# Optimization experiments

Hardware: AMD Instinct MI355X
Metric: run time of the kernel (lower is better)

Reference implementation:

```python
import jax, jax.numpy as jnp
import numpy as np

B, S, D, E, H = 1024, 256, 1024, 1024, 1024  # batch, state, belief, embedding, hidden
T1 = 32            # clip_length => number of scan steps
POSE_TILES = 4
MIN_STD = 0.1


def _gru(x, h, wih, whh, bih, bhh):
    # torch.nn.GRUCell semantics
    gi = x @ wih.T + bih
    gh = h @ whh.T + bhh
    i_r, i_z, i_n = jnp.split(gi, 3, axis=-1)
    h_r, h_z, h_n = jnp.split(gh, 3, axis=-1)
    r = jax.nn.sigmoid(i_r + h_r)
    z = jax.nn.sigmoid(i_z + h_z)
    n = jnp.tanh(i_n + r * h_n)
    return (1.0 - z) * n + z * h


def setup_inputs() -> dict:
    key = jax.random.key(0)
    ks = iter(jax.random.split(key, 40))
    g = lambda shape, s=1.0: jax.random.normal(next(ks), shape, dtype=jnp.float32) * s
    W = 0.02
    inp = {
        'prev_state': g((B, S)),
        'prev_belief': g((B, D)),
        'observations': g((T1, B, E)),
        'poses': g((T1, B, 6)),
        'noise_post': g((T1, B, S)),
        'noise_prior': g((T1, B, S)),
        # fc_embed_state_posterior: (2S+E) -> D
        'W_esq': g((D, 2 * S + E), W), 'b_esq': jnp.zeros((D,), jnp.float32),
        # fc_embed_state_prior: (2S+6*pose_tiles) -> D
        'W_esp': g((D, 2 * S + 6 * POSE_TILES), W), 'b_esp': jnp.zeros((D,), jnp.float32),
        # GRUCell posterior / prior
        'gq_wih': g((3 * D, D), W), 'gq_whh': g((3 * D, D), W),
        'gq_bih': jnp.zeros((3 * D,), jnp.float32), 'gq_bhh': jnp.zeros((3 * D,), jnp.float32),
        'gp_wih': g((3 * D, D), W), 'gp_whh': g((3 * D, D), W),
        'gp_bih': jnp.zeros((3 * D,), jnp.float32), 'gp_bhh': jnp.zeros((3 * D,), jnp.float32),
        # belief -> hidden -> 2*state heads
        'W_ebq': g((H, D), W), 'b_ebq': jnp.zeros((H,), jnp.float32),
        'W_sq': g((2 * S, H), W), 'b_sq': jnp.zeros((2 * S,), jnp.float32),
        'W_ebp': g((H, D), W), 'b_ebp': jnp.zeros((H,), jnp.float32),
        'W_sp': g((2 * S, H), W), 'b_sp': jnp.zeros((2 * S,), jnp.float32),
    }
    return inp


def reference(prev_state, prev_belief, observations, poses, noise_post, noise_prior,
              W_esq, b_esq, W_esp, b_esp,
              gq_wih, gq_whh, gq_bih, gq_bhh,
              gp_wih, gp_whh, gp_bih, gp_bhh,
              W_ebq, b_ebq, W_sq, b_sq, W_ebp, b_ebp, W_sp, b_sp):
    relu = jax.nn.relu

    def step(carry, xs):
        s_q, s_p, b_q, b_p = carry
        obs, pose, nq, npn = xs
        # posterior branch
        h = relu(jnp.concatenate([obs, s_q, s_p], axis=1) @ W_esq.T + b_esq)
        b_q_new = _gru(h, b_q, gq_wih, gq_whh, gq_bih, gq_bhh)
        hq = relu(b_q_new @ W_ebq.T + b_ebq)
        mq, raw_sq = jnp.split(hq @ W_sq.T + b_sq, 2, axis=1)
        std_q = jax.nn.softplus(raw_sq) + MIN_STD
        s_q_new = mq + std_q * nq
        # prior branch (uses old s_q, s_p per original code)
        pose_t = jnp.tile(pose, (1, POSE_TILES))
        h2 = relu(jnp.concatenate([pose_t, s_q, s_p], axis=1) @ W_esp.T + b_esp)
        b_p_new = _gru(h2, b_p, gp_wih, gp_whh, gp_bih, gp_bhh)
        hp = relu(b_p_new @ W_ebp.T + b_ebp)
        mp, raw_sp = jnp.split(hp @ W_sp.T + b_sp, 2, axis=1)
        std_p = jax.nn.softplus(raw_sp) + MIN_STD
        s_p_new = mp + std_p * npn
        new_carry = (s_q_new, s_p_new, b_q_new, b_p_new)
        ys = (b_q_new, s_p_new, mp, std_p, s_q_new, mq, std_q)
        return new_carry, ys

    carry0 = (prev_state, prev_state, prev_belief, prev_belief)
    _, ys = jax.lax.scan(step, carry0, (observations, poses, noise_post, noise_prior))
    post_beliefs, prior_states, prior_means, prior_stds, post_states, post_means, post_stds = ys
    # order matches torch: [posterior_beliefs, prior_states, prior_means, prior_std_devs,
    #                       posterior_states, posterior_means, posterior_std_devs]
    return (post_beliefs, prior_states, prior_means, prior_stds,
            post_states, post_means, post_stds)
```

## Files before the change

### kernel.cpp

```cpp
#include <hip/hip_runtime.h>
#include <stdint.h>
#include <math.h>

typedef unsigned short ushort_t;
typedef __attribute__((ext_vector_type(8))) short bf16x8;
typedef __attribute__((ext_vector_type(4))) float f32x4;

#define T1_ 32

#define SW_BAR() asm volatile("s_barrier" ::: "memory")
#define SW_VM(n) asm volatile("s_waitcnt vmcnt(" #n ")" ::: "memory")

__device__ __forceinline__ float bf2f(ushort_t u) {
  union { unsigned int i; float f; } v; v.i = ((unsigned int)u) << 16; return v.f;
}
__device__ __forceinline__ ushort_t f2bf(float f) {
  union { float f; unsigned int i; } v; v.f = f;
  unsigned int x = v.i;
  return (ushort_t)((x + 0x7FFFu + ((x >> 16) & 1u)) >> 16);
}
__device__ __forceinline__ float sigm(float x) { return 1.f / (1.f + expf(-x)); }

__device__ __forceinline__ void gld16(const ushort_t* g, ushort_t* l) {
  __builtin_amdgcn_global_load_lds(
      (const __attribute__((address_space(1))) unsigned int*)g,
      (__attribute__((address_space(3))) unsigned int*)l, 16, 0, 0);
}


__global__ __launch_bounds__(256) void cvt_k(const float* src, ushort_t* dst,
                                             long long n, int cols, int src_ld, int src_off) {
  const long long idx = (long long)blockIdx.x * 256 + threadIdx.x;
  if (idx >= n) return;
  const long long row = idx / cols;
  const int col = (int)(idx - row * cols);
  dst[idx] = f2bf(src[row * src_ld + src_off + col]);
}

__global__ __launch_bounds__(256) void wpe_k(const float* Wesp, float* wpe) {
  const int i = blockIdx.x * 256 + threadIdx.x;
  if (i >= 1024 * 6) return;
  const int n = i / 6, j = i % 6;
  float s = 0.f;
#pragma unroll
  for (int r = 0; r < 4; ++r) s += Wesp[(long long)n * 536 + j + 6 * r];
  wpe[i] = s;
}

__global__ void marker_k(float* out, float K) {
  if (threadIdx.x == 0 && blockIdx.x == 0) out[0] = K;
}

struct ObsqArgs { const ushort_t* A; const ushort_t* W; ushort_t* out; };
__global__ __launch_bounds__(256) void obsq_k(ObsqArgs g) {
  __shared__ __align__(16) ushort_t As[2][2048];
  __shared__ __align__(16) ushort_t Ws[2][4096];
  const int tid = threadIdx.x;
  const int lane = tid & 63, wv = tid >> 6;
  const int wm = wv >> 1, wn = wv & 1;
  const int bn0 = blockIdx.x * 128, bm0 = blockIdx.y * 64;
  const int srow = lane >> 2;
  const int sch8 = ((lane ^ (lane >> 2) ^ (lane >> 4)) & 3) * 8;
  const int rr = lane & 15, qq = lane >> 4;
  const int rslot8 = (((rr << 2) | ((qq ^ rr ^ (rr >> 2)) & 3)) * 8);

  f32x4 acc[2][4];
#pragma unroll
  for (int i = 0; i < 2; ++i)
#pragma unroll
    for (int j = 0; j < 4; ++j) acc[i][j] = (f32x4){0.f, 0.f, 0.f, 0.f};

  auto stage = [&](int buf, int kt) {
    const int k0 = kt * 32;
    gld16(g.A + (size_t)(bm0 + wv * 16 + srow) * 1024 + k0 + sch8, &As[buf][wv * 512]);
    gld16(g.W + (size_t)(bn0 + wv * 16 + srow) * 1536 + k0 + sch8, &Ws[buf][wv * 512]);
    gld16(g.W + (size_t)(bn0 + 64 + wv * 16 + srow) * 1536 + k0 + sch8,
          &Ws[buf][2048 + wv * 512]);
  };

  stage(0, 0);
  int cur = 0;
#pragma unroll 1
  for (int kt = 0; kt < 32; ++kt) {
    if (kt + 1 < 32) { stage(cur ^ 1, kt + 1); SW_VM(3); } else { SW_VM(0); }
    SW_BAR();
    bf16x8 a[2], b[4];
#pragma unroll
    for (int i = 0; i < 2; ++i)
      a[i] = *(const bf16x8*)&As[cur][(wm * 2 + i) * 512 + rslot8];
#pragma unroll
    for (int j = 0; j < 4; ++j)
      b[j] = *(const bf16x8*)&Ws[cur][(wn * 4 + j) * 512 + rslot8];
#pragma unroll
    for (int i = 0; i < 2; ++i)
#pragma unroll
      for (int j = 0; j < 4; ++j)
        acc[i][j] = __builtin_amdgcn_mfma_f32_16x16x32_bf16(a[i], b[j], acc[i][j], 0, 0, 0);
    if (kt + 1 < 32) SW_BAR();
    cur ^= 1;
  }

  const int r15 = lane & 15, rq = (lane >> 4) * 4;
#pragma unroll
  for (int i = 0; i < 2; ++i)
#pragma unroll
    for (int j = 0; j < 4; ++j) {
      const int col = bn0 + wn * 64 + j * 16 + r15;
#pragma unroll
      for (int q = 0; q < 4; ++q) {
        const int row = bm0 + wm * 32 + i * 16 + rq + q;
        g.out[(size_t)row * 1024 + col] = f2bf(acc[i][j][q]);
      }
    }
}

struct MMSide {
  const ushort_t* a0; const ushort_t* a1; const ushort_t* a2;
  int kd0, kd1, kd2;
  int coff0, coff1, coff2;
  const ushort_t* W; int ldw;
  const float* bias;
  ushort_t* outb;
  int dopose;
  const ushort_t* extrab;
};
struct MM2Args { MMSide s[2]; const float* poses_t; const float* wpe; };

__global__ __launch_bounds__(256) void mm2_k(MM2Args g) {
  const MMSide S = g.s[blockIdx.z];
  __shared__ __align__(16) ushort_t As[2][1024];
  __shared__ __align__(16) ushort_t Ws[2][4096];
  const int tid = threadIdx.x;
  const int lane = tid & 63, wv = tid >> 6;
  const int wn = wv;
  const int bn0 = blockIdx.x * 128, bm0 = blockIdx.y * 32;
  const int srow = lane >> 2;
  const int sch8 = ((lane ^ (lane >> 2) ^ (lane >> 4)) & 3) * 8;
  const int rr = lane & 15, qq = lane >> 4;
  const int rslot8 = (((rr << 2) | ((qq ^ rr ^ (rr >> 2)) & 3)) * 8);

  f32x4 acc[2][2];
#pragma unroll
  for (int i = 0; i < 2; ++i)
#pragma unroll
    for (int j = 0; j < 2; ++j) acc[i][j] = (f32x4){0.f, 0.f, 0.f, 0.f};

  const int nk0 = S.kd0 >> 5, nk1 = S.kd1 >> 5, nk2 = S.kd2 >> 5;
  const int c1 = nk0, c2 = nk0 + nk1, nkt = c2 + nk2;

  auto stage = [&](int buf, int ktg) {
    const ushort_t* ab; int ktl, kdim, cf;
    if (ktg < c1)      { ab = S.a0; ktl = ktg;      kdim = S.kd0; cf = S.coff0; }
    else if (ktg < c2) { ab = S.a1; ktl = ktg - c1; kdim = S.kd1; cf = S.coff1; }
    else               { ab = S.a2; ktl = ktg - c2; kdim = S.kd2; cf = S.coff2; }
    const int k0 = ktl * 32;
    gld16(S.W + cf + (size_t)(bn0 + wv * 16 + srow) * S.ldw + k0 + sch8, &Ws[buf][wv * 512]);
    gld16(S.W + cf + (size_t)(bn0 + 64 + wv * 16 + srow) * S.ldw + k0 + sch8,
          &Ws[buf][(wv + 4) * 512]);
    if (wv < 2)
      gld16(ab + (size_t)(bm0 + wv * 16 + srow) * kdim + k0 + sch8, &As[buf][wv * 512]);
  };

  stage(0, 0);
  int cur = 0;
#pragma unroll 1
  for (int ktg = 0; ktg < nkt; ++ktg) {
    if (ktg + 1 < nkt) {
      stage(cur ^ 1, ktg + 1);
      if (wv < 2) { SW_VM(3); } else { SW_VM(2); }
    } else { SW_VM(0); }
    SW_BAR();
    bf16x8 a[2], b[2];
#pragma unroll
    for (int i = 0; i < 2; ++i)
      a[i] = *(const bf16x8*)&As[cur][i * 512 + rslot8];
#pragma unroll
    for (int j = 0; j < 2; ++j)
      b[j] = *(const bf16x8*)&Ws[cur][(wn * 2 + j) * 512 + rslot8];
#pragma unroll
    for (int i = 0; i < 2; ++i)
#pragma unroll
      for (int j = 0; j < 2; ++j)
        acc[i][j] = __builtin_amdgcn_mfma_f32_16x16x32_bf16(a[i], b[j], acc[i][j], 0, 0, 0);
    if (ktg + 1 < nkt) SW_BAR();
    cur ^= 1;
  }

  const int r15 = lane & 15, rq = (lane >> 4) * 4;
#pragma unroll
  for (int i = 0; i < 2; ++i) {
#pragma unroll
    for (int j = 0; j < 2; ++j) {
      const int col = bn0 + wn * 32 + j * 16 + r15;
      const float bs = S.bias[col];
#pragma unroll
      for (int q = 0; q < 4; ++q) {
        const int row = bm0 + i * 16 + rq + q;
        float v = acc[i][j][q] + bs;
        if (S.extrab) v += bf2f(S.extrab[(size_t)row * 1024 + col]);
        if (S.dopose) {
          float s = 0.f;
#pragma unroll
          for (int jj = 0; jj < 6; ++jj)
            s += g.poses_t[(long long)row * 6 + jj] * g.wpe[col * 6 + jj];
          v += s;
        }
        v = fmaxf(v, 0.f);
        S.outb[(size_t)row * 1024 + col] = f2bf(v);
      }
    }
  }
}

struct GruSide {
  const ushort_t* x;
  const ushort_t* hb;
  const float* hf;
  const ushort_t* wih; const ushort_t* whh;
  const float* bih; const float* bhh;
  float* dst; ushort_t* dstb;
};
struct Gru2Args { GruSide s[2]; };

__global__ __launch_bounds__(256) void gru2_k(Gru2Args g) {
  const GruSide S = g.s[blockIdx.z];
  __shared__ __align__(16) ushort_t lds[2][16384];
  const int tid = threadIdx.x;
  const int lane = tid & 63, wv = tid >> 6;
  const int wm = wv >> 1, wn = wv & 1;
  const int bn0 = blockIdx.x * 64, bm0 = blockIdx.y * 64;
  const int srow = lane >> 2;
  const int sch8 = ((lane ^ (lane >> 2) ^ (lane >> 4)) & 3) * 8;
  const int rr = lane & 15, qq = lane >> 4;
  const int rslot8 = (((rr << 2) | ((qq ^ rr ^ (rr >> 2)) & 3)) * 8);

  f32x4 aR[2][2], aZ[2][2], aNI[2][2], aNH[2][2];
#pragma unroll
  for (int i = 0; i < 2; ++i)
#pragma unroll
    for (int j = 0; j < 2; ++j) {
      aR[i][j] = (f32x4){0.f,0.f,0.f,0.f}; aZ[i][j] = (f32x4){0.f,0.f,0.f,0.f};
      aNI[i][j] = (f32x4){0.f,0.f,0.f,0.f}; aNH[i][j] = (f32x4){0.f,0.f,0.f,0.f};
    }

  auto stage = [&](int buf, int kt) {
    const int k0 = kt * 32;
#pragma unroll
    for (int u = 0; u < 8; ++u) {
      const int G = wv * 8 + u;
      if (G < 4)
        gld16(S.x + (size_t)(bm0 + G * 16 + srow) * 1024 + k0 + sch8, &lds[buf][G * 512]);
      else if (G < 8)
        gld16(S.hb + (size_t)(bm0 + (G - 4) * 16 + srow) * 1024 + k0 + sch8, &lds[buf][G * 512]);
      else {
        const int wch = G - 8, gg = wch >> 2, rc = wch & 3;
        const ushort_t* base = (gg < 3) ? S.wih : S.whh;
        const int gr = (gg < 3 ? gg : gg - 3) * 1024 + bn0 + rc * 16 + srow;
        gld16(base + (size_t)gr * 1024 + k0 + sch8, &lds[buf][G * 512]);
      }
    }
  };

  stage(0, 0);
  int cur = 0;
#pragma unroll 1
  for (int kt = 0; kt < 32; ++kt) {
    if (kt + 1 < 32) { stage(cur ^ 1, kt + 1); SW_VM(8); } else { SW_VM(0); }
    SW_BAR();
    bf16x8 ax[2], ah[2], w[6][2];
#pragma unroll
    for (int i = 0; i < 2; ++i) {
      ax[i] = *(const bf16x8*)&lds[cur][(wm * 2 + i) * 512 + rslot8];
      ah[i] = *(const bf16x8*)&lds[cur][(4 + wm * 2 + i) * 512 + rslot8];
    }
#pragma unroll
    for (int gg = 0; gg < 6; ++gg)
#pragma unroll
      for (int j = 0; j < 2; ++j)
        w[gg][j] = *(const bf16x8*)&lds[cur][(8 + gg * 4 + wn * 2 + j) * 512 + rslot8];
#pragma unroll
    for (int i = 0; i < 2; ++i)
#pragma unroll
      for (int j = 0; j < 2; ++j) {
        aR[i][j]  = __builtin_amdgcn_mfma_f32_16x16x32_bf16(ax[i], w[0][j], aR[i][j], 0, 0, 0);
        aR[i][j]  = __builtin_amdgcn_mfma_f32_16x16x32_bf16(ah[i], w[3][j], aR[i][j], 0, 0, 0);
        aZ[i][j]  = __builtin_amdgcn_mfma_f32_16x16x32_bf16(ax[i], w[1][j], aZ[i][j], 0, 0, 0);
        aZ[i][j]  = __builtin_amdgcn_mfma_f32_16x16x32_bf16(ah[i], w[4][j], aZ[i][j], 0, 0, 0);
        aNI[i][j] = __builtin_amdgcn_mfma_f32_16x16x32_bf16(ax[i], w[2][j], aNI[i][j], 0, 0, 0);
        aNH[i][j] = __builtin_amdgcn_mfma_f32_16x16x32_bf16(ah[i], w[5][j], aNH[i][j], 0, 0, 0);
      }
    if (kt + 1 < 32) SW_BAR();
    cur ^= 1;
  }

  const int r15 = lane & 15, rq = (lane >> 4) * 4;
#pragma unroll
  for (int j = 0; j < 2; ++j) {
    const int col = bn0 + wn * 32 + j * 16 + r15;
    const float brz = S.bih[col] + S.bhh[col];
    const float bzz = S.bih[col + 1024] + S.bhh[col + 1024];
    const float bni = S.bih[col + 2048], bnh = S.bhh[col + 2048];
#pragma unroll
    for (int i = 0; i < 2; ++i) {
#pragma unroll
      for (int q = 0; q < 4; ++q) {
        const int row = bm0 + wm * 32 + i * 16 + rq + q;
        const float r = sigm(aR[i][j][q] + brz);
        const float z = sigm(aZ[i][j][q] + bzz);
        const float ng = tanhf(aNI[i][j][q] + bni + r * (aNH[i][j][q] + bnh));
        const size_t o = (size_t)row * 1024 + col;
        const float bnew = (1.f - z) * ng + z * S.hf[o];
        S.dst[o] = bnew;
        S.dstb[o] = f2bf(bnew);
      }
    }
  }
}

struct HeadSide {
  const ushort_t* hh;
  const ushort_t* Ws;
  const float* bs;
  const float* noise;
  float* omean; float* ostd; float* ostate;
  ushort_t* stateb;
};
struct Head2Args { HeadSide s[2]; };

__global__ __launch_bounds__(256) void head2_k(Head2Args g) {
  const HeadSide S = g.s[blockIdx.z];
  __shared__ __align__(16) ushort_t lds[2][3072];
  const int tid = threadIdx.x;
  const int lane = tid & 63, wv = tid >> 6;
  const int wm = wv >> 1, wn = wv & 1;
  const int bn0 = blockIdx.x * 32, bm0 = blockIdx.y * 32;
  const int srow = lane >> 2;
  const int sch8 = ((lane ^ (lane >> 2) ^ (lane >> 4)) & 3) * 8;
  const int rr = lane & 15, qq = lane >> 4;
  const int rslot8 = (((rr << 2) | ((qq ^ rr ^ (rr >> 2)) & 3)) * 8);

  f32x4 acc[2];
#pragma unroll
  for (int gg = 0; gg < 2; ++gg) acc[gg] = (f32x4){0.f, 0.f, 0.f, 0.f};

  auto stage = [&](int buf, int kt) {
    const int k0 = kt * 32;
    if (wv < 2) {
      gld16(S.hh + (size_t)(bm0 + wv * 16 + srow) * 1024 + k0 + sch8, &lds[buf][wv * 512]);
      gld16(S.Ws + (size_t)(bn0 + wv * 16 + srow) * 1024 + k0 + sch8, &lds[buf][(2 + wv) * 512]);
    } else {
      gld16(S.Ws + (size_t)(256 + bn0 + (wv - 2) * 16 + srow) * 1024 + k0 + sch8,
            &lds[buf][(2 + wv) * 512]);
    }
  };

  stage(0, 0);
  int cur = 0;
#pragma unroll 1
  for (int kt = 0; kt < 32; ++kt) {
    if (kt + 1 < 32) {
      stage(cur ^ 1, kt + 1);
      if (wv < 2) { SW_VM(2); } else { SW_VM(1); }
    } else { SW_VM(0); }
    SW_BAR();
    const bf16x8 a = *(const bf16x8*)&lds[cur][wm * 512 + rslot8];
    const bf16x8 w0 = *(const bf16x8*)&lds[cur][(2 + wn) * 512 + rslot8];
    const bf16x8 w1 = *(const bf16x8*)&lds[cur][(4 + wn) * 512 + rslot8];
    acc[0] = __builtin_amdgcn_mfma_f32_16x16x32_bf16(a, w0, acc[0], 0, 0, 0);
    acc[1] = __builtin_amdgcn_mfma_f32_16x16x32_bf16(a, w1, acc[1], 0, 0, 0);
    if (kt + 1 < 32) SW_BAR();
    cur ^= 1;
  }

  const int r15 = lane & 15, rq = (lane >> 4) * 4;
  const int col = bn0 + wn * 16 + r15;
  const float bm_ = S.bs[col];
  const float bsd = S.bs[col + 256];
#pragma unroll
  for (int q = 0; q < 4; ++q) {
    const int row = bm0 + wm * 16 + rq + q;
    const float mean = acc[0][q] + bm_;
    const float rs = acc[1][q] + bsd;
    const float sp = fmaxf(rs, 0.f) + log1pf(expf(-fabsf(rs)));
    const float sd = sp + 0.1f;
    const long long o = (long long)row * 256 + col;
    const float st = mean + sd * S.noise[o];
    S.omean[o] = mean; S.ostd[o] = sd; S.ostate[o] = st;
    S.stateb[o] = f2bf(st);
  }
}

extern "C" void kernel_launch(void* const* d_in, const int* in_sizes, int n_in,
                              void* d_out, int out_size, void* d_ws, size_t ws_size,
                              hipStream_t stream) {
  float* out = (float*)d_out;

  int gid = 0;
  if (n_in != 26) gid = 1;
  else if (out_size != 83886080) gid = 2;
  else if (in_sizes[0] != 262144 || in_sizes[1] != 1048576 || in_sizes[2] != 33554432 ||
           in_sizes[3] != 196608 || in_sizes[4] != 8388608 || in_sizes[5] != 8388608) gid = 3;
  else if (in_sizes[6] != 1572864 || in_sizes[8] != 548864) gid = 4;
  else if (in_sizes[10] != 3145728 || in_sizes[11] != 3145728 ||
           in_sizes[14] != 3145728 || in_sizes[15] != 3145728) gid = 5;
  else if (in_sizes[18] != 1048576 || in_sizes[20] != 524288 ||
           in_sizes[22] != 1048576 || in_sizes[24] != 524288) gid = 6;
  else if (ws_size < (184ull << 20)) gid = 7;
  if (gid != 0) {
    unsigned wsMB = (unsigned)(ws_size >> 20); if (wsMB > 4095u) wsMB = 4095u;
    const float K = (float)gid * 16777216.0f + (float)wsMB;
    hipLaunchKernelGGL(marker_k, dim3(1), dim3(64), 0, stream, out, K);
    return;
  }

  const float* prev_state  = (const float*)d_in[0];
  const float* prev_belief = (const float*)d_in[1];
  const float* observations= (const float*)d_in[2];
  const float* poses       = (const float*)d_in[3];
  const float* noise_post  = (const float*)d_in[4];
  const float* noise_prior = (const float*)d_in[5];
  const float* W_esq = (const float*)d_in[6];  const float* b_esq = (const float*)d_in[7];
  const float* W_esp = (const float*)d_in[8];  const float* b_esp = (const float*)d_in[9];
  const float* gq_wih = (const float*)d_in[10]; const float* gq_whh = (const float*)d_in[11];
  const float* gq_bih = (const float*)d_in[12]; const float* gq_bhh = (const float*)d_in[13];
  const float* gp_wih = (const float*)d_in[14]; const float* gp_whh = (const float*)d_in[15];
  const float* gp_bih = (const float*)d_in[16]; const float* gp_bhh = (const float*)d_in[17];
  const float* W_ebq = (const float*)d_in[18]; const float* b_ebq = (const float*)d_in[19];
  const float* W_sq  = (const float*)d_in[20]; const float* b_sq  = (const float*)d_in[21];
  const float* W_ebp = (const float*)d_in[22]; const float* b_ebp = (const float*)d_in[23];
  const float* W_sp  = (const float*)d_in[24]; const float* b_sp  = (const float*)d_in[25];

  float* out_belief = out;
  float* out_pstate = out + 33554432LL;
  float* out_pmean  = out + 41943040LL;
  float* out_pstd   = out + 50331648LL;
  float* out_qstate = out + 58720256LL;
  float* out_qmean  = out + 67108864LL;
  float* out_qstd   = out + 75497472LL;

  char* w = (char*)d_ws;
  ushort_t* obsb  = (ushort_t*)(w);
  ushort_t* OBSQ  = (ushort_t*)(w + (64ull << 20));
  ushort_t* wWesq = (ushort_t*)(w + (128ull << 20));
  ushort_t* wWesp = (ushort_t*)(w + (131ull << 20));
  ushort_t* wGqih = (ushort_t*)(w + (132ull << 20));
  ushort_t* wGqhh = (ushort_t*)(w + (138ull << 20));
  ushort_t* wGpih = (ushort_t*)(w + (144ull << 20));
  ushort_t* wGphh = (ushort_t*)(w + (150ull << 20));
  ushort_t* wEbq  = (ushort_t*)(w + (156ull << 20));
  ushort_t* wEbp  = (ushort_t*)(w + (158ull << 20));
  ushort_t* wSq   = (ushort_t*)(w + (160ull << 20));
  ushort_t* wSp   = (ushort_t*)(w + (161ull << 20));
  float*    wpe   = (float*)(w + (162ull << 20));
  ushort_t* h_q   = (ushort_t*)(w + (163ull << 20));
  ushort_t* h_p   = (ushort_t*)(w + (165ull << 20));
  ushort_t* bqb[2] = { (ushort_t*)(w + (167ull << 20)), (ushort_t*)(w + (169ull << 20)) };
  ushort_t* bpb[2] = { (ushort_t*)(w + (171ull << 20)), (ushort_t*)(w + (173ull << 20)) };
  ushort_t* sqb   = (ushort_t*)(w + (175ull << 20));
  ushort_t* spb   = (ushort_t*)(w + (175ull << 20) + 524288);
  float*    bpf[2] = { (float*)(w + (176ull << 20)), (float*)(w + (180ull << 20)) };

  const dim3 blk(256);
  auto cvt = [&](const float* s, ushort_t* d, long long n, int c, int ld, int off) {
    hipLaunchKernelGGL(cvt_k, dim3((unsigned)((n + 255) / 256)), blk, 0, stream, s, d, n, c, ld, off);
  };
  cvt(observations, obsb, 33554432LL, 1024, 1024, 0);
  cvt(W_esq, wWesq, 1572864LL, 1536, 1536, 0);
  cvt(W_esp, wWesp, 524288LL, 512, 536, 24);
  cvt(gq_wih, wGqih, 3145728LL, 1024, 1024, 0);
  cvt(gq_whh, wGqhh, 3145728LL, 1024, 1024, 0);
  cvt(gp_wih, wGpih, 3145728LL, 1024, 1024, 0);
  cvt(gp_whh, wGphh, 3145728LL, 1024, 1024, 0);
  cvt(W_ebq, wEbq, 1048576LL, 1024, 1024, 0);
  cvt(W_ebp, wEbp, 1048576LL, 1024, 1024, 0);
  cvt(W_sq, wSq, 524288LL, 1024, 1024, 0);
  cvt(W_sp, wSp, 524288LL, 1024, 1024, 0);
  cvt(prev_state, sqb, 262144LL, 256, 256, 0);
  cvt(prev_state, spb, 262144LL, 256, 256, 0);
  cvt(prev_belief, bqb[1], 1048576LL, 1024, 1024, 0);
  cvt(prev_belief, bpb[1], 1048576LL, 1024, 1024, 0);
  hipLaunchKernelGGL(wpe_k, dim3(24), blk, 0, stream, W_esp, wpe);

  {
    ObsqArgs oa{ obsb, wWesq, OBSQ };
    hipLaunchKernelGGL(obsq_k, dim3(8, 512), blk, 0, stream, oa);
  }

  for (int t = 0; t < T1_; ++t) {
    const int cur = t & 1, prv = cur ^ 1;
    const float* bq_prev_f = (t == 0) ? prev_belief : out_belief + (long long)(t - 1) * 1048576;
    const float* bp_prev_f = (t == 0) ? prev_belief : bpf[prv];

    MM2Args a{};
    a.s[0] = MMSide{ sqb, spb, nullptr, 256, 256, 0, 1024, 1280, 0,
                     wWesq, 1536, b_esq, h_q, 0, OBSQ + (long long)t * 1048576 };
    a.s[1] = MMSide{ sqb, spb, nullptr, 256, 256, 0, 0, 256, 0,
                     wWesp, 512, b_esp, h_p, 1, nullptr };
    a.poses_t = poses + (long long)t * 6144; a.wpe = wpe;
    hipLaunchKernelGGL(mm2_k, dim3(8, 32, 2), blk, 0, stream, a);

    Gru2Args gr{};
    gr.s[0] = GruSide{ h_q, bqb[prv], bq_prev_f, wGqih, wGqhh, gq_bih, gq_bhh,
                       out_belief + (long long)t * 1048576, bqb[cur] };
    gr.s[1] = GruSide{ h_p, bpb[prv], bp_prev_f, wGpih, wGphh, gp_bih, gp_bhh,
                       bpf[cur], bpb[cur] };
    hipLaunchKernelGGL(gru2_k, dim3(16, 16, 2), blk, 0, stream, gr);

    a = MM2Args{};
    a.s[0] = MMSide{ bqb[cur], nullptr, nullptr, 1024, 0, 0, 0, 0, 0,
                     wEbq, 1024, b_ebq, h_q, 0, nullptr };
    a.s[1] = MMSide{ bpb[cur], nullptr, nullptr, 1024, 0, 0, 0, 0, 0,
                     wEbp, 1024, b_ebp, h_p, 0, nullptr };
    hipLaunchKernelGGL(mm2_k, dim3(8, 32, 2), blk, 0, stream, a);

    Head2Args hd{};
    hd.s[0] = HeadSide{ h_q, wSq, b_sq, noise_post + (long long)t * 262144,
                        out_qmean + (long long)t * 262144,
                        out_qstd + (long long)t * 262144,
                        out_qstate + (long long)t * 262144, sqb };
    hd.s[1] = HeadSide{ h_p, wSp, b_sp, noise_prior + (long long)t * 262144,
                        out_pmean + (long long)t * 262144,
                        out_pstd + (long long)t * 262144,
                        out_pstate + (long long)t * 262144, spb };
    hipLaunchKernelGGL(head2_k, dim3(8, 32, 2), blk, 0, stream, hd);
  }
}
```

Before: 3.440 ms.

## Fuse the recurrent scan into one persistent cooperative kernel with grid syncs

```diff
diff --git a/kernel.cpp b/kernel.cpp
--- a/kernel.cpp
+++ b/kernel.cpp
@@ -1,13 +1,15 @@
 #include <hip/hip_runtime.h>
+#include <hip/hip_cooperative_groups.h>
 #include <stdint.h>
 #include <math.h>
+
+namespace cg = cooperative_groups;
 
 typedef unsigned short ushort_t;
 typedef __attribute__((ext_vector_type(8))) short bf16x8;
 typedef __attribute__((ext_vector_type(4))) float f32x4;
 
 #define T1_ 32
-
 #define SW_BAR() asm volatile("s_barrier" ::: "memory")
 #define SW_VM(n) asm volatile("s_waitcnt vmcnt(" #n ")" ::: "memory")
 
@@ -115,9 +117,9 @@
 }
 
 struct MMSide {
-  const ushort_t* a0; const ushort_t* a1; const ushort_t* a2;
-  int kd0, kd1, kd2;
-  int coff0, coff1, coff2;
+  const ushort_t* a0; const ushort_t* a1;
+  int kd0, kd1;
+  int coff0, coff1;
   const ushort_t* W; int ldw;
   const float* bias;
   ushort_t* outb;
@@ -145,14 +147,12 @@
 #pragma unroll
     for (int j = 0; j < 2; ++j) acc[i][j] = (f32x4){0.f, 0.f, 0.f, 0.f};
 
-  const int nk0 = S.kd0 >> 5, nk1 = S.kd1 >> 5, nk2 = S.kd2 >> 5;
-  const int c1 = nk0, c2 = nk0 + nk1, nkt = c2 + nk2;
+  const int nk0 = S.kd0 >> 5, nkt = nk0 + (S.kd1 >> 5);
 
   auto stage = [&](int buf, int ktg) {
     const ushort_t* ab; int ktl, kdim, cf;
-    if (ktg < c1)      { ab = S.a0; ktl = ktg;      kdim = S.kd0; cf = S.coff0; }
-    else if (ktg < c2) { ab = S.a1; ktl = ktg - c1; kdim = S.kd1; cf = S.coff1; }
-    else               { ab = S.a2; ktl = ktg - c2; kdim = S.kd2; cf = S.coff2; }
+    if (ktg < nk0) { ab = S.a0; ktl = ktg;       kdim = S.kd0; cf = S.coff0; }
+    else           { ab = S.a1; ktl = ktg - nk0; kdim = S.kd1; cf = S.coff1; }
     const int k0 = ktl * 32;
     gld16(S.W + cf + (size_t)(bn0 + wv * 16 + srow) * S.ldw + k0 + sch8, &Ws[buf][wv * 512]);
     gld16(S.W + cf + (size_t)(bn0 + 64 + wv * 16 + srow) * S.ldw + k0 + sch8,
@@ -340,8 +340,8 @@
   const int rslot8 = (((rr << 2) | ((qq ^ rr ^ (rr >> 2)) & 3)) * 8);
 
   f32x4 acc[2];
-#pragma unroll
-  for (int gg = 0; gg < 2; ++gg) acc[gg] = (f32x4){0.f, 0.f, 0.f, 0.f};
+  acc[0] = (f32x4){0.f, 0.f, 0.f, 0.f};
+  acc[1] = (f32x4){0.f, 0.f, 0.f, 0.f};
 
   auto stage = [&](int buf, int kt) {
     const int k0 = kt * 32;
@@ -390,6 +390,344 @@
   }
 }
 
+struct CoopArgs {
+  const ushort_t *OBSQ, *wWesq, *wWesp, *wGqih, *wGqhh, *wGpih, *wGphh,
+                 *wEbq, *wEbp, *wSq, *wSp;
+  const float *b_esq, *b_esp, *gq_bih, *gq_bhh, *gp_bih, *gp_bhh,
+              *b_ebq, *b_ebp, *b_sq, *b_sp;
+  const float *poses, *noise_q, *noise_p, *prev_belief, *wpe;
+  ushort_t *h_q, *h_p, *bqb0, *bqb1, *bpb0, *bpb1, *sqb, *spb;
+  float *bpf0, *bpf1;
+  float* out;
+};
+
+__global__ __launch_bounds__(512, 2) void scan2_k(CoopArgs A) {
+  cg::grid_group grid = cg::this_grid();
+  __shared__ __align__(16) ushort_t ldsAll[2][2][16384];
+  const int bid = blockIdx.x, tid = threadIdx.x;
+  const int z = tid >> 8;
+  const int ltid = tid & 255;
+  const int lane = ltid & 63, wv = ltid >> 6;
+  const int srow = lane >> 2;
+  const int sch8 = ((lane ^ (lane >> 2) ^ (lane >> 4)) & 3) * 8;
+  const int rr = lane & 15, qq = lane >> 4;
+  const int rslot8 = (((rr << 2) | ((qq ^ rr ^ (rr >> 2)) & 3)) * 8);
+  const int r15 = lane & 15, rq = (lane >> 4) * 4;
+  ushort_t (*lds)[16384] = ldsAll[z];
+
+  ushort_t* bqb[2] = { A.bqb0, A.bqb1 };
+  ushort_t* bpb[2] = { A.bpb0, A.bpb1 };
+  float* bpf[2] = { A.bpf0, A.bpf1 };
+
+  for (int t = 0; t < T1_; ++t) {
+    const int cur = t & 1, prv = cur ^ 1;
+
+    {
+      const int bn0 = (bid & 7) * 128, bm0 = ((bid >> 3) & 31) * 32;
+      const int wn = wv;
+      const ushort_t* Wp; int ldw, cf0, cf1, dopose;
+      const float* bias; ushort_t* outb; const ushort_t* extrab;
+      if (z == 0) { Wp = A.wWesq; ldw = 1536; cf0 = 1024; cf1 = 1280; dopose = 0;
+                    bias = A.b_esq; outb = A.h_q; extrab = A.OBSQ + (size_t)t * 1048576; }
+      else        { Wp = A.wWesp; ldw = 512;  cf0 = 0;    cf1 = 256;  dopose = 1;
+                    bias = A.b_esp; outb = A.h_p; extrab = nullptr; }
+      f32x4 acc[2][2];
+#pragma unroll
+      for (int i = 0; i < 2; ++i)
+#pragma unroll
+        for (int j = 0; j < 2; ++j) acc[i][j] = (f32x4){0.f, 0.f, 0.f, 0.f};
+
+      auto stage = [&](int buf, int ktg) {
+        const ushort_t* ab = (ktg < 8) ? A.sqb : A.spb;
+        const int cf = (ktg < 8) ? cf0 : cf1;
+        const int k0 = (ktg & 7) * 32;
+        gld16(Wp + cf + (size_t)(bn0 + wv * 16 + srow) * ldw + k0 + sch8,
+              &lds[buf][1024 + wv * 512]);
+        gld16(Wp + cf + (size_t)(bn0 + 64 + wv * 16 + srow) * ldw + k0 + sch8,
+              &lds[buf][1024 + (wv + 4) * 512]);
+        if (wv < 2)
+          gld16(ab + (size_t)(bm0 + wv * 16 + srow) * 256 + k0 + sch8, &lds[buf][wv * 512]);
+      };
+
+      stage(0, 0);
+      int cb = 0;
+#pragma unroll 1
+      for (int ktg = 0; ktg < 16; ++ktg) {
+        if (ktg + 1 < 16) { stage(cb ^ 1, ktg + 1); if (wv < 2) { SW_VM(3); } else { SW_VM(2); } }
+        else { SW_VM(0); }
+        SW_BAR();
+        bf16x8 a[2], b[2];
+#pragma unroll
+        for (int i = 0; i < 2; ++i)
+          a[i] = *(const bf16x8*)&lds[cb][i * 512 + rslot8];
+#pragma unroll
+        for (int j = 0; j < 2; ++j)
+          b[j] = *(const bf16x8*)&lds[cb][1024 + (wn * 2 + j) * 512 + rslot8];
+#pragma unroll
+        for (int i = 0; i < 2; ++i)
+#pragma unroll
+          for (int j = 0; j < 2; ++j)
+            acc[i][j] = __builtin_amdgcn_mfma_f32_16x16x32_bf16(a[i], b[j], acc[i][j], 0, 0, 0);
+        if (ktg + 1 < 16) SW_BAR();
+        cb ^= 1;
+      }
+
+      const float* poses_t = A.poses + (size_t)t * 6144;
+#pragma unroll
+      for (int i = 0; i < 2; ++i) {
+#pragma unroll
+        for (int j = 0; j < 2; ++j) {
+          const int col = bn0 + wn * 32 + j * 16 + r15;
+          const float bs = bias[col];
+#pragma unroll
+          for (int q = 0; q < 4; ++q) {
+            const int row = bm0 + i * 16 + rq + q;
+            float v = acc[i][j][q] + bs;
+            if (extrab) v += bf2f(extrab[(size_t)row * 1024 + col]);
+            if (dopose) {
+              float s = 0.f;
+#pragma unroll
+              for (int jj = 0; jj < 6; ++jj)
+                s += poses_t[(size_t)row * 6 + jj] * A.wpe[col * 6 + jj];
+              v += s;
+            }
+            v = fmaxf(v, 0.f);
+            outb[(size_t)row * 1024 + col] = f2bf(v);
+          }
+        }
+      }
+    }
+    grid.sync();
+
+    {
+      const int bn0 = (bid & 15) * 64, bm0 = ((bid >> 4) & 15) * 64;
+      const int wm = wv >> 1, wn = wv & 1;
+      const ushort_t *x, *hb, *wih, *whh;
+      const float *hf, *bih, *bhh;
+      float* dst; ushort_t* dstb;
+      if (z == 0) {
+        x = A.h_q; hb = bqb[prv];
+        hf = t ? (A.out + (size_t)(t - 1) * 1048576) : A.prev_belief;
+        wih = A.wGqih; whh = A.wGqhh; bih = A.gq_bih; bhh = A.gq_bhh;
+        dst = A.out + (size_t)t * 1048576; dstb = bqb[cur];
+      } else {
+        x = A.h_p; hb = bpb[prv];
+        hf = t ? bpf[prv] : A.prev_belief;
+        wih = A.wGpih; whh = A.wGphh; bih = A.gp_bih; bhh = A.gp_bhh;
+        dst = bpf[cur]; dstb = bpb[cur];
+      }
+
+      f32x4 aR[2][2], aZ[2][2], aNI[2][2], aNH[2][2];
+#pragma unroll
+      for (int i = 0; i < 2; ++i)
+#pragma unroll
+        for (int j = 0; j < 2; ++j) {
+          aR[i][j] = (f32x4){0.f,0.f,0.f,0.f}; aZ[i][j] = (f32x4){0.f,0.f,0.f,0.f};
+          aNI[i][j] = (f32x4){0.f,0.f,0.f,0.f}; aNH[i][j] = (f32x4){0.f,0.f,0.f,0.f};
+        }
+
+      auto stage = [&](int buf, int kt) {
+        const int k0 = kt * 32;
+#pragma unroll
+        for (int u = 0; u < 8; ++u) {
+          const int G = wv * 8 + u;
+          if (G < 4)
+            gld16(x + (size_t)(bm0 + G * 16 + srow) * 1024 + k0 + sch8, &lds[buf][G * 512]);
+          else if (G < 8)
+            gld16(hb + (size_t)(bm0 + (G - 4) * 16 + srow) * 1024 + k0 + sch8, &lds[buf][G * 512]);
+          else {
+            const int wch = G - 8, gg = wch >> 2, rc = wch & 3;
+            const ushort_t* base = (gg < 3) ? wih : whh;
+            const int gr = (gg < 3 ? gg : gg - 3) * 1024 + bn0 + rc * 16 + srow;
+            gld16(base + (size_t)gr * 1024 + k0 + sch8, &lds[buf][G * 512]);
+          }
+        }
+      };
+
+      stage(0, 0);
+      int cb = 0;
+#pragma unroll 1
+      for (int kt = 0; kt < 32; ++kt) {
+        if (kt + 1 < 32) { stage(cb ^ 1, kt + 1); SW_VM(8); } else { SW_VM(0); }
+        SW_BAR();
+        bf16x8 ax[2], ah[2], w[6][2];
+#pragma unroll
+        for (int i = 0; i < 2; ++i) {
+          ax[i] = *(const bf16x8*)&lds[cb][(wm * 2 + i) * 512 + rslot8];
+          ah[i] = *(const bf16x8*)&lds[cb][(4 + wm * 2 + i) * 512 + rslot8];
+        }
+#pragma unroll
+        for (int gg = 0; gg < 6; ++gg)
+#pragma unroll
+          for (int j = 0; j < 2; ++j)
+            w[gg][j] = *(const bf16x8*)&lds[cb][(8 + gg * 4 + wn * 2 + j) * 512 + rslot8];
+#pragma unroll
+        for (int i = 0; i < 2; ++i)
+#pragma unroll
+          for (int j = 0; j < 2; ++j) {
+            aR[i][j]  = __builtin_amdgcn_mfma_f32_16x16x32_bf16(ax[i], w[0][j], aR[i][j], 0, 0, 0);
+            aR[i][j]  = __builtin_amdgcn_mfma_f32_16x16x32_bf16(ah[i], w[3][j], aR[i][j], 0, 0, 0);
+            aZ[i][j]  = __builtin_amdgcn_mfma_f32_16x16x32_bf16(ax[i], w[1][j], aZ[i][j], 0, 0, 0);
+            aZ[i][j]  = __builtin_amdgcn_mfma_f32_16x16x32_bf16(ah[i], w[4][j], aZ[i][j], 0, 0, 0);
+            aNI[i][j] = __builtin_amdgcn_mfma_f32_16x16x32_bf16(ax[i], w[2][j], aNI[i][j], 0, 0, 0);
+            aNH[i][j] = __builtin_amdgcn_mfma_f32_16x16x32_bf16(ah[i], w[5][j], aNH[i][j], 0, 0, 0);
+          }
+        if (kt + 1 < 32) SW_BAR();
+        cb ^= 1;
+      }
+
+#pragma unroll
+      for (int j = 0; j < 2; ++j) {
+        const int col = bn0 + wn * 32 + j * 16 + r15;
+        const float brz = bih[col] + bhh[col];
+        const float bzz = bih[col + 1024] + bhh[col + 1024];
+        const float bni = bih[col + 2048], bnh = bhh[col + 2048];
+#pragma unroll
+        for (int i = 0; i < 2; ++i) {
+#pragma unroll
+          for (int q = 0; q < 4; ++q) {
+            const int row = bm0 + wm * 32 + i * 16 + rq + q;
+            const float r = sigm(aR[i][j][q] + brz);
+            const float zz = sigm(aZ[i][j][q] + bzz);
+            const float ng = tanhf(aNI[i][j][q] + bni + r * (aNH[i][j][q] + bnh));
+            const size_t o = (size_t)row * 1024 + col;
+            const float bnew = (1.f - zz) * ng + zz * hf[o];
+            dst[o] = bnew;
+            dstb[o] = f2bf(bnew);
+          }
+        }
+      }
+    }
+    grid.sync();
+
+    {
+      const int bn0 = (bid & 7) * 128, bm0 = ((bid >> 3) & 31) * 32;
+      const int wn = wv;
+      const ushort_t* ab = (z == 0) ? bqb[cur] : bpb[cur];
+      const ushort_t* Wp = (z == 0) ? A.wEbq : A.wEbp;
+      const float* bias = (z == 0) ? A.b_ebq : A.b_ebp;
+      ushort_t* outb = (z == 0) ? A.h_q : A.h_p;
+
+      f32x4 acc[2][2];
+#pragma unroll
+      for (int i = 0; i < 2; ++i)
+#pragma unroll
+        for (int j = 0; j < 2; ++j) acc[i][j] = (f32x4){0.f, 0.f, 0.f, 0.f};
+
+      auto stage = [&](int buf, int kt) {
+        const int k0 = kt * 32;
+        gld16(Wp + (size_t)(bn0 + wv * 16 + srow) * 1024 + k0 + sch8,
+              &lds[buf][1024 + wv * 512]);
+        gld16(Wp + (size_t)(bn0 + 64 + wv * 16 + srow) * 1024 + k0 + sch8,
+              &lds[buf][1024 + (wv + 4) * 512]);
+        if (wv < 2)
+          gld16(ab + (size_t)(bm0 + wv * 16 + srow) * 1024 + k0 + sch8, &lds[buf][wv * 512]);
+      };
+
+      stage(0, 0);
+      int cb = 0;
+#pragma unroll 1
+      for (int kt = 0; kt < 32; ++kt) {
+        if (kt + 1 < 32) { stage(cb ^ 1, kt + 1); if (wv < 2) { SW_VM(3); } else { SW_VM(2); } }
+        else { SW_VM(0); }
+        SW_BAR();
+        bf16x8 a[2], b[2];
+#pragma unroll
+        for (int i = 0; i < 2; ++i)
+          a[i] = *(const bf16x8*)&lds[cb][i * 512 + rslot8];
+#pragma unroll
+        for (int j = 0; j < 2; ++j)
+          b[j] = *(const bf16x8*)&lds[cb][1024 + (wn * 2 + j) * 512 + rslot8];
+#pragma unroll
+        for (int i = 0; i < 2; ++i)
+#pragma unroll
+          for (int j = 0; j < 2; ++j)
+            acc[i][j] = __builtin_amdgcn_mfma_f32_16x16x32_bf16(a[i], b[j], acc[i][j], 0, 0, 0);
+        if (kt + 1 < 32) SW_BAR();
+        cb ^= 1;
+      }
+
+#pragma unroll
+      for (int i = 0; i < 2; ++i) {
+#pragma unroll
+        for (int j = 0; j < 2; ++j) {
+          const int col = bn0 + wn * 32 + j * 16 + r15;
+          const float bs = bias[col];
+#pragma unroll
+          for (int q = 0; q < 4; ++q) {
+            const int row = bm0 + i * 16 + rq + q;
+            const float v = fmaxf(acc[i][j][q] + bs, 0.f);
+            outb[(size_t)row * 1024 + col] = f2bf(v);
+          }
+        }
+      }
+    }
+    grid.sync();
+
+    {
+      const int bn0 = (bid & 7) * 32, bm0 = ((bid >> 3) & 31) * 32;
+      const int wm = wv >> 1, wn = wv & 1;
+      const ushort_t* hh = (z == 0) ? A.h_q : A.h_p;
+      const ushort_t* Ws = (z == 0) ? A.wSq : A.wSp;
+      const float* bs = (z == 0) ? A.b_sq : A.b_sp;
+      const float* noise = ((z == 0) ? A.noise_q : A.noise_p) + (size_t)t * 262144;
+      float* omean  = A.out + ((z == 0) ? 67108864LL : 41943040LL) + (size_t)t * 262144;
+      float* ostd   = A.out + ((z == 0) ? 75497472LL : 50331648LL) + (size_t)t * 262144;
+      float* ostate = A.out + ((z == 0) ? 58720256LL : 33554432LL) + (size_t)t * 262144;
+      ushort_t* stb = (z == 0) ? A.sqb : A.spb;
+
+      f32x4 acc[2];
+      acc[0] = (f32x4){0.f, 0.f, 0.f, 0.f};
+      acc[1] = (f32x4){0.f, 0.f, 0.f, 0.f};
+
+      auto stage = [&](int buf, int kt) {
+        const int k0 = kt * 32;
+        if (wv < 2) {
+          gld16(hh + (size_t)(bm0 + wv * 16 + srow) * 1024 + k0 + sch8, &lds[buf][wv * 512]);
+          gld16(Ws + (size_t)(bn0 + wv * 16 + srow) * 1024 + k0 + sch8,
+                &lds[buf][(2 + wv) * 512]);
+        } else {
+          gld16(Ws + (size_t)(256 + bn0 + (wv - 2) * 16 + srow) * 1024 + k0 + sch8,
+                &lds[buf][(2 + wv) * 512]);
+        }
+      };
+
+      stage(0, 0);
+      int cb = 0;
+#pragma unroll 1
+      for (int kt = 0; kt < 32; ++kt) {
+        if (kt + 1 < 32) { stage(cb ^ 1, kt + 1); if (wv < 2) { SW_VM(2); } else { SW_VM(1); } }
+        else { SW_VM(0); }
+        SW_BAR();
+        const bf16x8 a = *(const bf16x8*)&lds[cb][wm * 512 + rslot8];
+        const bf16x8 w0 = *(const bf16x8*)&lds[cb][(2 + wn) * 512 + rslot8];
+        const bf16x8 w1 = *(const bf16x8*)&lds[cb][(4 + wn) * 512 + rslot8];
+        acc[0] = __builtin_amdgcn_mfma_f32_16x16x32_bf16(a, w0, acc[0], 0, 0, 0);
+        acc[1] = __builtin_amdgcn_mfma_f32_16x16x32_bf16(a, w1, acc[1], 0, 0, 0);
+        if (kt + 1 < 32) SW_BAR();
+        cb ^= 1;
+      }
+
+      const int col = bn0 + wn * 16 + r15;
+      const float bm_ = bs[col];
+      const float bsd = bs[col + 256];
+#pragma unroll
+      for (int q = 0; q < 4; ++q) {
+        const int row = bm0 + wm * 16 + rq + q;
+        const float mean = acc[0][q] + bm_;
+        const float rs = acc[1][q] + bsd;
+        const float sp = fmaxf(rs, 0.f) + log1pf(expf(-fabsf(rs)));
+        const float sd = sp + 0.1f;
+        const long long o = (long long)row * 256 + col;
+        const float st = mean + sd * noise[o];
+        omean[o] = mean; ostd[o] = sd; ostate[o] = st;
+        stb[o] = f2bf(st);
+      }
+    }
+    grid.sync();
+  }
+}
+
 extern "C" void kernel_launch(void* const* d_in, const int* in_sizes, int n_in,
                               void* d_out, int out_size, void* d_ws, size_t ws_size,
                               hipStream_t stream) {
@@ -454,11 +792,14 @@
   float*    wpe   = (float*)(w + (162ull << 20));
   ushort_t* h_q   = (ushort_t*)(w + (163ull << 20));
   ushort_t* h_p   = (ushort_t*)(w + (165ull << 20));
-  ushort_t* bqb[2] = { (ushort_t*)(w + (167ull << 20)), (ushort_t*)(w + (169ull << 20)) };
-  ushort_t* bpb[2] = { (ushort_t*)(w + (171ull << 20)), (ushort_t*)(w + (173ull << 20)) };
+  ushort_t* bqb0  = (ushort_t*)(w + (167ull << 20));
+  ushort_t* bqb1  = (ushort_t*)(w + (169ull << 20));
+  ushort_t* bpb0  = (ushort_t*)(w + (171ull << 20));
+  ushort_t* bpb1  = (ushort_t*)(w + (173ull << 20));
   ushort_t* sqb   = (ushort_t*)(w + (175ull << 20));
   ushort_t* spb   = (ushort_t*)(w + (175ull << 20) + 524288);
-  float*    bpf[2] = { (float*)(w + (176ull << 20)), (float*)(w + (180ull << 20)) };
+  float*    bpf0  = (float*)(w + (176ull << 20));
+  float*    bpf1  = (float*)(w + (180ull << 20));
 
   const dim3 blk(256);
   auto cvt = [&](const float* s, ushort_t* d, long long n, int c, int ld, int off) {
@@ -477,8 +818,8 @@
   cvt(W_sp, wSp, 524288LL, 1024, 1024, 0);
   cvt(prev_state, sqb, 262144LL, 256, 256, 0);
   cvt(prev_state, spb, 262144LL, 256, 256, 0);
-  cvt(prev_belief, bqb[1], 1048576LL, 1024, 1024, 0);
-  cvt(prev_belief, bpb[1], 1048576LL, 1024, 1024, 0);
+  cvt(prev_belief, bqb1, 1048576LL, 1024, 1024, 0);
+  cvt(prev_belief, bpb1, 1048576LL, 1024, 1024, 0);
   hipLaunchKernelGGL(wpe_k, dim3(24), blk, 0, stream, W_esp, wpe);
 
   {
@@ -486,15 +827,37 @@
     hipLaunchKernelGGL(obsq_k, dim3(8, 512), blk, 0, stream, oa);
   }
 
+  CoopArgs A{};
+  A.OBSQ = OBSQ; A.wWesq = wWesq; A.wWesp = wWesp;
+  A.wGqih = wGqih; A.wGqhh = wGqhh; A.wGpih = wGpih; A.wGphh = wGphh;
+  A.wEbq = wEbq; A.wEbp = wEbp; A.wSq = wSq; A.wSp = wSp;
+  A.b_esq = b_esq; A.b_esp = b_esp;
+  A.gq_bih = gq_bih; A.gq_bhh = gq_bhh; A.gp_bih = gp_bih; A.gp_bhh = gp_bhh;
+  A.b_ebq = b_ebq; A.b_ebp = b_ebp; A.b_sq = b_sq; A.b_sp = b_sp;
+  A.poses = poses; A.noise_q = noise_post; A.noise_p = noise_prior;
+  A.prev_belief = prev_belief; A.wpe = wpe;
+  A.h_q = h_q; A.h_p = h_p;
+  A.bqb0 = bqb0; A.bqb1 = bqb1; A.bpb0 = bpb0; A.bpb1 = bpb1;
+  A.sqb = sqb; A.spb = spb; A.bpf0 = bpf0; A.bpf1 = bpf1;
+  A.out = out;
+
+  void* params[] = { (void*)&A };
+  hipError_t cerr = hipLaunchCooperativeKernel((const void*)scan2_k, dim3(256), dim3(512),
+                                               params, 0, stream);
+  if (cerr == hipSuccess) return;
+
+  ushort_t* bqb[2] = { bqb0, bqb1 };
+  ushort_t* bpb[2] = { bpb0, bpb1 };
+  float* bpf[2] = { bpf0, bpf1 };
   for (int t = 0; t < T1_; ++t) {
     const int cur = t & 1, prv = cur ^ 1;
     const float* bq_prev_f = (t == 0) ? prev_belief : out_belief + (long long)(t - 1) * 1048576;
     const float* bp_prev_f = (t == 0) ? prev_belief : bpf[prv];
 
     MM2Args a{};
-    a.s[0] = MMSide{ sqb, spb, nullptr, 256, 256, 0, 1024, 1280, 0,
+    a.s[0] = MMSide{ sqb, spb, 256, 256, 1024, 1280,
                      wWesq, 1536, b_esq, h_q, 0, OBSQ + (long long)t * 1048576 };
-    a.s[1] = MMSide{ sqb, spb, nullptr, 256, 256, 0, 0, 256, 0,
+    a.s[1] = MMSide{ sqb, spb, 256, 256, 0, 256,
                      wWesp, 512, b_esp, h_p, 1, nullptr };
     a.poses_t = poses + (long long)t * 6144; a.wpe = wpe;
     hipLaunchKernelGGL(mm2_k, dim3(8, 32, 2), blk, 0, stream, a);
@@ -507,9 +870,9 @@
     hipLaunchKernelGGL(gru2_k, dim3(16, 16, 2), blk, 0, stream, gr);
 
     a = MM2Args{};
-    a.s[0] = MMSide{ bqb[cur], nullptr, nullptr, 1024, 0, 0, 0, 0, 0,
+    a.s[0] = MMSide{ bqb[cur], bqb[cur], 1024, 0, 0, 0,
                      wEbq, 1024, b_ebq, h_q, 0, nullptr };
-    a.s[1] = MMSide{ bpb[cur], nullptr, nullptr, 1024, 0, 0, 0, 0, 0,
+    a.s[1] = MMSide{ bpb[cur], bpb[cur], 1024, 0, 0, 0,
                      wEbp, 1024, b_ebp, h_p, 0, nullptr };
     hipLaunchKernelGGL(mm2_k, dim3(8, 32, 2), blk, 0, stream, a);
 
```

Result: slower. 7.760 ms (+125.6%).
